# Kernel tuning notes

Hardware: AMD Instinct MI355X
Metric: run time of the kernel (lower is better)

## Reference

```python
import jax, jax.numpy as jnp
import numpy as np

N, D_IN, D_OUT, NHEAD = 4096, 512, 128, 4


def setup_inputs() -> dict:
    key = jax.random.key(0)
    k1, k2, k3, k4, k5 = jax.random.split(key, 5)
    adj = jax.random.randint(k1, (N, N), 0, 2).astype(jnp.float32)  # dense binary adjacency
    x = jax.random.normal(k2, (N, D_IN), dtype=jnp.float32)
    W = jax.random.normal(k3, (D_IN, D_OUT), dtype=jnp.float32) * (1.0 / np.sqrt(D_IN))
    attn_l_w = jax.random.normal(k4, (NHEAD, D_OUT), dtype=jnp.float32) * (1.0 / np.sqrt(D_OUT))
    attn_r_w = jax.random.normal(k5, (NHEAD, D_OUT), dtype=jnp.float32) * (1.0 / np.sqrt(D_OUT))
    b = jnp.zeros((D_OUT,), dtype=jnp.float32)
    return {"adj": adj, "x": x, "W": W, "attn_l_w": attn_l_w, "attn_r_w": attn_r_w, "b": b}


def reference(adj, x, W, attn_l_w, attn_r_w, b):
    # h = x @ W : [N, D_OUT]
    h = x @ W
    el = h @ attn_l_w.T  # [N, H]  (nn.Linear(output_dim, nhead, bias=False))
    er = h @ attn_r_w.T  # [N, H]
    # Dense equivalent of nonzero-gather + index_put_ scatter into [N, N, H]:
    # attn[i, j, :] = exp(leaky_relu(el[i] + er[j])) where adj[i, j] != 0, else 0.
    e = el[:, None, :] + er[None, :, :]                      # [N, N, H]
    a = jnp.where(adj[:, :, None] != 0,
                  jnp.exp(jax.nn.leaky_relu(e, negative_slope=0.2)),
                  jnp.zeros((), dtype=e.dtype))              # [N, N, H]
    a = jnp.transpose(a, (0, 2, 1))                          # [N, H, N]
    # F.normalize(p=1, dim=-1): divide by max(L1 row sum, 1e-12); a >= 0 so L1 = sum.
    a = a / jnp.maximum(jnp.sum(a, axis=-1, keepdims=True), 1e-12)
    out = jnp.einsum('nhm,md->nhd', a, h) + b                # [N, H, D_OUT]
    return out.reshape(out.shape[0], -1)                     # flatten heads -> [N, H*D_OUT]
```

## Files before the change

kernel.cpp:

```cpp
#include <hip/hip_runtime.h>

#define NN 4096
#define DIN 512
#define DOUT 128
#define NH 4
#define LOG2E 1.44269504088896340736f

typedef __bf16 bf16x8 __attribute__((ext_vector_type(8)));
typedef float f32x4 __attribute__((ext_vector_type(4)));
typedef unsigned short u16;
typedef u16 u16x8 __attribute__((ext_vector_type(8)));
typedef unsigned long long u64;

static __device__ __forceinline__ u16 f2bf(float f) {
  __bf16 h = (__bf16)f;
  return __builtin_bit_cast(u16, h);
}

__global__ __launch_bounds__(256) void pack_adj(const float* __restrict__ adj,
                                                u64* __restrict__ adjW) {
  const int t = threadIdx.x;
  const int lane = t & 63;
  const int wv = t >> 6;
  const size_t blk = blockIdx.x;
  #pragma unroll
  for (int it = 0; it < 4; ++it) {
    const size_t wbase = blk * 128 + it * 32 + wv * 8;
    float v[8];
    #pragma unroll
    for (int u = 0; u < 8; ++u) v[u] = adj[(wbase + u) * 64 + lane];
    #pragma unroll
    for (int u = 0; u < 8; ++u) {
      const u64 m = __ballot(v[u] != 0.0f);
      if (lane == 0) adjW[wbase + u] = m;
    }
  }
}

__global__ __launch_bounds__(256) void prep_wt(const float* __restrict__ W,
                                               u16* __restrict__ wthi,
                                               u16* __restrict__ wtlo) {
  const int n = blockIdx.x;
  const int t = threadIdx.x;
  for (int k = t; k < 512; k += 256) {
    const float w = W[(size_t)k * 128 + n];
    const __bf16 hi = (__bf16)w;
    const float lo = w - (float)hi;
    wthi[(size_t)n * 512 + k] = __builtin_bit_cast(u16, hi);
    wtlo[(size_t)n * 512 + k] = f2bf(lo);
  }
}

__global__ __launch_bounds__(256, 2) void hcompute(
    const float* __restrict__ x, const u16* __restrict__ wthi,
    const u16* __restrict__ wtlo, const float* __restrict__ alw,
    const float* __restrict__ arw, u16* __restrict__ hT,
    float* __restrict__ el, float* __restrict__ erT) {
  __shared__ __align__(16) char pool[73728];
  float* h_lds = (float*)(pool + 8192);
  const int t = threadIdx.x;
  const int i0 = blockIdx.x * 16;
  const int lane = t & 63, wv = t >> 6;
  const int l15 = lane & 15, lhi = lane >> 4;
  f32x4 acc[2];
  #pragma unroll
  for (int nt = 0; nt < 2; ++nt) acc[nt] = (f32x4){0.f, 0.f, 0.f, 0.f};
  const int xr = t >> 4, xq = (t & 15) * 8;
  const unsigned x_waddr = (unsigned)(xr * 256 + xq * 2) ^ (unsigned)((xr & 7) << 4);
  const int wn = t >> 1, wkh = (t & 1) * 64;

  for (int kc = 0; kc < 4; ++kc) {
    __syncthreads();
    {
      const float* xsrc = x + (size_t)(i0 + xr) * DIN + kc * 128 + xq;
      float xv[8];
      *(float4*)xv = *(const float4*)xsrc;
      *(float4*)(xv + 4) = *(const float4*)(xsrc + 4);
      u16x8 xhi, xlo;
      #pragma unroll
      for (int q = 0; q < 8; ++q) {
        const __bf16 hh = (__bf16)xv[q];
        xhi[q] = __builtin_bit_cast(u16, hh);
        xlo[q] = f2bf(xv[q] - (float)hh);
      }
      *(u16x8*)(pool + x_waddr) = xhi;
      *(u16x8*)(pool + 4096 + x_waddr) = xlo;
    }
    {
      const u16* whsrc = wthi + (size_t)wn * 512 + kc * 128 + wkh;
      const u16* wlsrc = wtlo + (size_t)wn * 512 + kc * 128 + wkh;
      #pragma unroll
      for (int q = 0; q < 8; ++q) {
        const unsigned addr =
            (unsigned)(wn * 256 + (wkh + q * 8) * 2) ^ (unsigned)((wn & 7) << 4);
        *(u16x8*)(pool + 8192 + addr) = *(const u16x8*)(whsrc + q * 8);
        *(u16x8*)(pool + 40960 + addr) = *(const u16x8*)(wlsrc + q * 8);
      }
    }
    __syncthreads();
    #pragma unroll
    for (int ks = 0; ks < 4; ++ks) {
      const unsigned kbyte = (unsigned)(ks * 64 + lhi * 16);
      const unsigned xoff = (unsigned)(l15 * 256) + (kbyte ^ (unsigned)((l15 & 7) << 4));
      const bf16x8 ah = *(const bf16x8*)(pool + xoff);
      const bf16x8 al = *(const bf16x8*)(pool + 4096 + xoff);
      #pragma unroll
      for (int nt = 0; nt < 2; ++nt) {
        const int n = wv * 32 + nt * 16 + l15;
        const unsigned wb = (unsigned)(n * 256) + (kbyte ^ (unsigned)((n & 7) << 4));
        const bf16x8 bh = *(const bf16x8*)(pool + 8192 + wb);
        const bf16x8 bl = *(const bf16x8*)(pool + 40960 + wb);
        acc[nt] = __builtin_amdgcn_mfma_f32_16x16x32_bf16(ah, bh, acc[nt], 0, 0, 0);
        acc[nt] = __builtin_amdgcn_mfma_f32_16x16x32_bf16(al, bh, acc[nt], 0, 0, 0);
        acc[nt] = __builtin_amdgcn_mfma_f32_16x16x32_bf16(ah, bl, acc[nt], 0, 0, 0);
      }
    }
  }
  __syncthreads();
  #pragma unroll
  for (int nt = 0; nt < 2; ++nt)
    #pragma unroll
    for (int reg = 0; reg < 4; ++reg)
      h_lds[(lhi * 4 + reg) * 132 + wv * 32 + nt * 16 + l15] = acc[nt][reg];
  __syncthreads();
  {
    const int d = t >> 1, ih = (t & 1) * 8;
    u16x8 hv;
    #pragma unroll
    for (int q = 0; q < 8; ++q) hv[q] = f2bf(h_lds[(ih + q) * 132 + d]);
    *(u16x8*)(hT + (size_t)d * NN + i0 + ih) = hv;
  }
  if (t < 128) {
    const int r = t >> 3, hh = (t >> 1) & 3, side = t & 1;
    const float* wrow = (side ? arw : alw) + hh * DOUT;
    float s = 0.f;
    for (int d = 0; d < 128; ++d) s += h_lds[r * 132 + d] * wrow[d];
    s *= LOG2E;
    if (side == 0) el[(size_t)(i0 + r) * NH + hh] = s;
    else erT[(size_t)hh * NN + i0 + r] = s;
  }
}

template <int KSPLIT>
__global__ __launch_bounds__(512, 4) void gat_main(
    const unsigned char* __restrict__ adjB, const u16* __restrict__ hT,
    const float* __restrict__ el, const float* __restrict__ erT,
    const float* __restrict__ bias, float* __restrict__ outp,
    float* __restrict__ accP, float* __restrict__ SP) {
  constexpr int NIT = 64 / KSPLIT;
  __shared__ __align__(16) u16 A_lds[2][64 * 64];
  __shared__ __align__(16) u16 B_lds[2][128 * 64];
  __shared__ float S_lds[64];
  const int t = threadIdx.x;
  const int b = blockIdx.x;
  const int g = b & 255;
  const int ks = (KSPLIT > 1) ? (b >> 8) : 0;
  const int i0 = g * 16;
  const int row = t >> 3, head = row >> 4, il = row & 15;
  const int j0 = (t & 7) * 8;
  const float elv = el[(size_t)(i0 + il) * NH + head];
  const unsigned char* adjrow =
      adjB + (size_t)(i0 + il) * 512 + (size_t)ks * NIT * 8 + (t & 7);
  const float* errow = erT + (size_t)head * NN + ks * NIT * 64 + j0;
  const unsigned a_off = (unsigned)(row * 128 + j0 * 2) ^ (unsigned)((row & 7) << 4);
  const int bd = t >> 3, bk0 = (t & 7) * 8;
  const u16* hrow = hT + (size_t)bd * NN + ks * NIT * 64 + bk0;
  const unsigned b_off0 = (unsigned)(bd * 128 + bk0 * 2) ^ (unsigned)((bd & 7) << 4);
  const unsigned b_off1 =
      (unsigned)((bd + 64) * 128 + bk0 * 2) ^ (unsigned)((bd & 7) << 4);
  const int lane = t & 63, w = t >> 6;
  const int rt = w >> 1, ch = w & 1;
  const int l15 = lane & 15, lhi = lane >> 4;
  const int am = rt * 16 + l15;
  const unsigned aswz = (unsigned)((am & 7) << 4);
  f32x4 acc[4];
  #pragma unroll
  for (int ct = 0; ct < 4; ++ct) acc[ct] = (f32x4){0.f, 0.f, 0.f, 0.f};
  float Sp = 0.f;

  auto genTile = [&](unsigned char abv, const float4& ea, const float4& eb,
                     char* Abuf, char* Bbuf, const u16x8& h0, const u16x8& h1) {
    float ev[8];
    *(float4*)ev = ea;
    *(float4*)(ev + 4) = eb;
    u16x8 pk;
    float s = 0.f;
    #pragma unroll
    for (int q = 0; q < 8; ++q) {
      const float e = elv + ev[q];
      const float ex = exp2f(fmaxf(e, 0.f) + 0.2f * fminf(e, 0.f));
      const float av = (float)((abv >> q) & 1) * ex;
      s += av;
      pk[q] = f2bf(av);
    }
    Sp += s;
    *(u16x8*)(Abuf + a_off) = pk;
    *(u16x8*)(Bbuf + b_off0) = h0;
    *(u16x8*)(Bbuf + b_off1) = h1;
  };

  {
    const unsigned char ab = adjrow[0];
    const float4 e0 = *(const float4*)errow;
    const float4 e1 = *(const float4*)(errow + 4);
    const u16x8 h0 = *(const u16x8*)hrow;
    const u16x8 h1 = *(const u16x8*)(hrow + (size_t)64 * NN);
    genTile(ab, e0, e1, (char*)A_lds[0], (char*)B_lds[0], h0, h1);
  }

  for (int jt = 0; jt < NIT; ++jt) {
    const int cur = jt & 1;
    __syncthreads();
    unsigned char abn = 0;
    float4 e0n, e1n;
    u16x8 h0n, h1n;
    const bool more = (jt + 1 < NIT);
    if (more) {
      abn = adjrow[(jt + 1) * 8];
      e0n = *(const float4*)(errow + (jt + 1) * 64);
      e1n = *(const float4*)(errow + (jt + 1) * 64 + 4);
      h0n = *(const u16x8*)(hrow + (jt + 1) * 64);
      h1n = *(const u16x8*)(hrow + (jt + 1) * 64 + (size_t)64 * NN);
    }
    const char* Abc = (const char*)A_lds[cur];
    const char* Bbc = (const char*)B_lds[cur];
    #pragma unroll
    for (int kk = 0; kk < 2; ++kk) {
      const unsigned kbyte = (unsigned)(kk * 64 + lhi * 16);
      const bf16x8 af = *(const bf16x8*)(Abc + (am * 128 + (kbyte ^ aswz)));
      #pragma unroll
      for (int ct = 0; ct < 4; ++ct) {
        const int col = ch * 64 + ct * 16 + l15;
        const bf16x8 bfr = *(const bf16x8*)(
            Bbc + (col * 128 + (kbyte ^ (unsigned)((col & 7) << 4))));
        acc[ct] = __builtin_amdgcn_mfma_f32_16x16x32_bf16(af, bfr, acc[ct], 0, 0, 0);
      }
    }
    if (more)
      genTile(abn, e0n, e1n, (char*)A_lds[cur ^ 1], (char*)B_lds[cur ^ 1], h0n, h1n);
  }

  Sp += __shfl_xor(Sp, 1);
  Sp += __shfl_xor(Sp, 2);
  Sp += __shfl_xor(Sp, 4);

  if (KSPLIT == 1) {
    if ((t & 7) == 0) S_lds[row] = Sp;
    __syncthreads();
    #pragma unroll
    for (int reg = 0; reg < 4; ++reg) {
      const int mrow = rt * 16 + lhi * 4 + reg;
      const float inv = 1.f / fmaxf(S_lds[mrow], 1e-12f);
      const int irow = i0 + (mrow & 15);
      #pragma unroll
      for (int ct = 0; ct < 4; ++ct) {
        const int colp = ch * 64 + ct * 16 + l15;
        outp[(size_t)irow * (NH * DOUT) + rt * DOUT + colp] =
            acc[ct][reg] * inv + bias[colp];
      }
    }
  } else {
    if ((t & 7) == 0) SP[(size_t)b * 64 + row] = Sp;
    float* dst = accP + (size_t)b * 8192;
    #pragma unroll
    for (int reg = 0; reg < 4; ++reg) {
      const int mrow = rt * 16 + lhi * 4 + reg;
      #pragma unroll
      for (int ct = 0; ct < 4; ++ct) {
        const int colp = ch * 64 + ct * 16 + l15;
        dst[mrow * 128 + colp] = acc[ct][reg];
      }
    }
  }
}

__global__ __launch_bounds__(256) void reduce_norm(
    const float* __restrict__ accP, const float* __restrict__ SP,
    const float* __restrict__ bias, float* __restrict__ outp) {
  const int idx = blockIdx.x * 256 + threadIdx.x;
  const int o = idx * 4;
  const int d = o & 127;
  const int h = (o >> 7) & 3;
  const int i = o >> 9;
  const int g = i >> 4;
  const int m = h * 16 + (i & 15);
  const float4 p0 = *(const float4*)(accP + (size_t)g * 8192 + m * 128 + d);
  const float4 p1 = *(const float4*)(accP + (size_t)(256 + g) * 8192 + m * 128 + d);
  const float S = SP[(size_t)g * 64 + m] + SP[(size_t)(256 + g) * 64 + m];
  const float inv = 1.f / fmaxf(S, 1e-12f);
  const float4 bb = *(const float4*)(bias + d);
  float4 r;
  r.x = (p0.x + p1.x) * inv + bb.x;
  r.y = (p0.y + p1.y) * inv + bb.y;
  r.z = (p0.z + p1.z) * inv + bb.z;
  r.w = (p0.w + p1.w) * inv + bb.w;
  *(float4*)(outp + o) = r;
}

extern "C" void kernel_launch(void* const* d_in, const int* in_sizes, int n_in,
                              void* d_out, int out_size, void* d_ws, size_t ws_size,
                              hipStream_t stream) {
  const float* adj = (const float*)d_in[0];
  const float* x = (const float*)d_in[1];
  const float* W = (const float*)d_in[2];
  const float* alw = (const float*)d_in[3];
  const float* arw = (const float*)d_in[4];
  const float* bias = (const float*)d_in[5];
  float* out = (float*)d_out;
  char* ws = (char*)d_ws;
  u16* hT = (u16*)ws;
  float* el = (float*)(ws + 0x100000);
  float* erT = (float*)(ws + 0x110000);
  unsigned char* adjB = (unsigned char*)(ws + 0x120000);
  u16* wthi = (u16*)(ws + 0x320000);
  u16* wtlo = (u16*)(ws + 0x340000);
  float* accP = (float*)(ws + 0x360000);
  float* SP = (float*)(ws + 0x1360000);
  const bool ksplit2 = ws_size >= 0x1380000ull;

  pack_adj<<<2048, 256, 0, stream>>>(adj, (u64*)adjB);
  prep_wt<<<128, 256, 0, stream>>>(W, wthi, wtlo);
  hcompute<<<256, 256, 0, stream>>>(x, wthi, wtlo, alw, arw, hT, el, erT);
  if (ksplit2) {
    gat_main<2><<<512, 512, 0, stream>>>(adjB, hT, el, erT, bias, out, accP, SP);
    reduce_norm<<<2048, 256, 0, stream>>>(accP, SP, bias, out);
  } else {
    gat_main<1><<<256, 512, 0, stream>>>(adjB, hT, el, erT, bias, out, accP, SP);
  }
}
```

Before: 177.3 us.

## Async global-to-LDS staging, 3-way K split, and branchless leaky-relu mask

The main GAT kernel now stages the hT tiles straight into LDS with global_load_lds instead of going through registers. It also splits the neighbour dimension three ways when the workspace allows, giving 768 blocks instead of 512 for better CU fill. Leaky-relu becomes a single fma on |e| and the adjacency mask is applied with a bitwise AND instead of a multiply. hcompute moves to 512 threads, double-buffers W through direct LDS loads, and prefetches the next x chunk. The 3-way split adds partial-sum traffic in reduce_norm and needs more workspace.

```diff
diff --git a/kernel.cpp b/kernel.cpp
--- a/kernel.cpp
+++ b/kernel.cpp
@@ -10,11 +10,18 @@
 typedef float f32x4 __attribute__((ext_vector_type(4)));
 typedef unsigned short u16;
 typedef u16 u16x8 __attribute__((ext_vector_type(8)));
+typedef u16 u16x4 __attribute__((ext_vector_type(4)));
 typedef unsigned long long u64;
 
 static __device__ __forceinline__ u16 f2bf(float f) {
   __bf16 h = (__bf16)f;
   return __builtin_bit_cast(u16, h);
+}
+
+static __device__ __forceinline__ void gl_lds16(const void* g, void* l) {
+  __builtin_amdgcn_global_load_lds(
+      (const __attribute__((address_space(1))) unsigned int*)g,
+      (__attribute__((address_space(3))) unsigned int*)l, 16, 0, 0);
 }
 
 __global__ __launch_bounds__(256) void pack_adj(const float* __restrict__ adj,
@@ -51,84 +58,92 @@
   }
 }
 
-__global__ __launch_bounds__(256, 2) void hcompute(
+__global__ __launch_bounds__(512, 1) void hcompute(
     const float* __restrict__ x, const u16* __restrict__ wthi,
     const u16* __restrict__ wtlo, const float* __restrict__ alw,
     const float* __restrict__ arw, u16* __restrict__ hT,
     float* __restrict__ el, float* __restrict__ erT) {
-  __shared__ __align__(16) char pool[73728];
-  float* h_lds = (float*)(pool + 8192);
+  __shared__ __align__(16) char pool[147456];
   const int t = threadIdx.x;
   const int i0 = blockIdx.x * 16;
-  const int lane = t & 63, wv = t >> 6;
+  const int lane = t & 63, w = t >> 6;
   const int l15 = lane & 15, lhi = lane >> 4;
-  f32x4 acc[2];
-  #pragma unroll
-  for (int nt = 0; nt < 2; ++nt) acc[nt] = (f32x4){0.f, 0.f, 0.f, 0.f};
-  const int xr = t >> 4, xq = (t & 15) * 8;
-  const unsigned x_waddr = (unsigned)(xr * 256 + xq * 2) ^ (unsigned)((xr & 7) << 4);
-  const int wn = t >> 1, wkh = (t & 1) * 64;
-
+
+  const int xr = t >> 5, xk = (t & 31) * 4;
+  const unsigned x_off =
+      ((unsigned)(xr * 256 + xk * 2)) ^ ((unsigned)((xr & 7) << 4));
+
+  f32x4 acc = (f32x4){0.f, 0.f, 0.f, 0.f};
+
+  auto stageW = [&](int kc, int buf) {
+    #pragma unroll
+    for (int q = 0; q < 4; ++q) {
+      const int off = q * 8192 + t * 16;
+      const int n = off >> 8;
+      const int kb = off & 255;
+      const int ksrc = (kb ^ ((n & 7) << 4)) >> 1;
+      const size_t so = (size_t)n * 512 + kc * 128 + ksrc;
+      gl_lds16(wthi + so, pool + 16384 + buf * 32768 + off);
+      gl_lds16(wtlo + so, pool + 81920 + buf * 32768 + off);
+    }
+  };
+  auto writeX = [&](const float4& xv, int buf) {
+    u16x4 hi, lo;
+    const float* xp = (const float*)&xv;
+    #pragma unroll
+    for (int j = 0; j < 4; ++j) {
+      const __bf16 hb = (__bf16)xp[j];
+      hi[j] = __builtin_bit_cast(u16, hb);
+      lo[j] = f2bf(xp[j] - (float)hb);
+    }
+    *(u16x4*)(pool + buf * 4096 + x_off) = hi;
+    *(u16x4*)(pool + 8192 + buf * 4096 + x_off) = lo;
+  };
+
+  stageW(0, 0);
+  {
+    float4 xv = *(const float4*)(x + (size_t)(i0 + xr) * DIN + xk);
+    writeX(xv, 0);
+  }
+  float4 xnext;
   for (int kc = 0; kc < 4; ++kc) {
+    const int cur = kc & 1;
     __syncthreads();
-    {
-      const float* xsrc = x + (size_t)(i0 + xr) * DIN + kc * 128 + xq;
-      float xv[8];
-      *(float4*)xv = *(const float4*)xsrc;
-      *(float4*)(xv + 4) = *(const float4*)(xsrc + 4);
-      u16x8 xhi, xlo;
-      #pragma unroll
-      for (int q = 0; q < 8; ++q) {
-        const __bf16 hh = (__bf16)xv[q];
-        xhi[q] = __builtin_bit_cast(u16, hh);
-        xlo[q] = f2bf(xv[q] - (float)hh);
-      }
-      *(u16x8*)(pool + x_waddr) = xhi;
-      *(u16x8*)(pool + 4096 + x_waddr) = xlo;
-    }
-    {
-      const u16* whsrc = wthi + (size_t)wn * 512 + kc * 128 + wkh;
-      const u16* wlsrc = wtlo + (size_t)wn * 512 + kc * 128 + wkh;
-      #pragma unroll
-      for (int q = 0; q < 8; ++q) {
-        const unsigned addr =
-            (unsigned)(wn * 256 + (wkh + q * 8) * 2) ^ (unsigned)((wn & 7) << 4);
-        *(u16x8*)(pool + 8192 + addr) = *(const u16x8*)(whsrc + q * 8);
-        *(u16x8*)(pool + 40960 + addr) = *(const u16x8*)(wlsrc + q * 8);
-      }
-    }
-    __syncthreads();
+    const bool more = (kc < 3);
+    if (more) {
+      stageW(kc + 1, cur ^ 1);
+      xnext = *(const float4*)(x + (size_t)(i0 + xr) * DIN + (kc + 1) * 128 + xk);
+    }
     #pragma unroll
     for (int ks = 0; ks < 4; ++ks) {
       const unsigned kbyte = (unsigned)(ks * 64 + lhi * 16);
-      const unsigned xoff = (unsigned)(l15 * 256) + (kbyte ^ (unsigned)((l15 & 7) << 4));
-      const bf16x8 ah = *(const bf16x8*)(pool + xoff);
-      const bf16x8 al = *(const bf16x8*)(pool + 4096 + xoff);
-      #pragma unroll
-      for (int nt = 0; nt < 2; ++nt) {
-        const int n = wv * 32 + nt * 16 + l15;
-        const unsigned wb = (unsigned)(n * 256) + (kbyte ^ (unsigned)((n & 7) << 4));
-        const bf16x8 bh = *(const bf16x8*)(pool + 8192 + wb);
-        const bf16x8 bl = *(const bf16x8*)(pool + 40960 + wb);
-        acc[nt] = __builtin_amdgcn_mfma_f32_16x16x32_bf16(ah, bh, acc[nt], 0, 0, 0);
-        acc[nt] = __builtin_amdgcn_mfma_f32_16x16x32_bf16(al, bh, acc[nt], 0, 0, 0);
-        acc[nt] = __builtin_amdgcn_mfma_f32_16x16x32_bf16(ah, bl, acc[nt], 0, 0, 0);
-      }
-    }
+      const unsigned xoff =
+          (unsigned)(l15 * 256) + (kbyte ^ (unsigned)((l15 & 7) << 4));
+      const bf16x8 ah = *(const bf16x8*)(pool + cur * 4096 + xoff);
+      const bf16x8 al = *(const bf16x8*)(pool + 8192 + cur * 4096 + xoff);
+      const int n = w * 16 + l15;
+      const unsigned wb =
+          (unsigned)(n * 256) + (kbyte ^ (unsigned)((n & 7) << 4));
+      const bf16x8 bh = *(const bf16x8*)(pool + 16384 + cur * 32768 + wb);
+      const bf16x8 bl = *(const bf16x8*)(pool + 81920 + cur * 32768 + wb);
+      acc = __builtin_amdgcn_mfma_f32_16x16x32_bf16(ah, bh, acc, 0, 0, 0);
+      acc = __builtin_amdgcn_mfma_f32_16x16x32_bf16(al, bh, acc, 0, 0, 0);
+      acc = __builtin_amdgcn_mfma_f32_16x16x32_bf16(ah, bl, acc, 0, 0, 0);
+    }
+    if (more) writeX(xnext, cur ^ 1);
   }
   __syncthreads();
+  float* h_lds = (float*)(pool + 16384);
   #pragma unroll
-  for (int nt = 0; nt < 2; ++nt)
-    #pragma unroll
-    for (int reg = 0; reg < 4; ++reg)
-      h_lds[(lhi * 4 + reg) * 132 + wv * 32 + nt * 16 + l15] = acc[nt][reg];
+  for (int reg = 0; reg < 4; ++reg)
+    h_lds[(lhi * 4 + reg) * 132 + w * 16 + l15] = acc[reg];
   __syncthreads();
   {
-    const int d = t >> 1, ih = (t & 1) * 8;
-    u16x8 hv;
-    #pragma unroll
-    for (int q = 0; q < 8; ++q) hv[q] = f2bf(h_lds[(ih + q) * 132 + d]);
-    *(u16x8*)(hT + (size_t)d * NN + i0 + ih) = hv;
+    const int d = t >> 2, ih0 = (t & 3) * 4;
+    u16x4 hv;
+    #pragma unroll
+    for (int j = 0; j < 4; ++j) hv[j] = f2bf(h_lds[(ih0 + j) * 132 + d]);
+    *(u16x4*)(hT + (size_t)d * NN + i0 + ih0) = hv;
   }
   if (t < 128) {
     const int r = t >> 3, hh = (t >> 1) & 3, side = t & 1;
@@ -147,7 +162,6 @@
     const float* __restrict__ el, const float* __restrict__ erT,
     const float* __restrict__ bias, float* __restrict__ outp,
     float* __restrict__ accP, float* __restrict__ SP) {
-  constexpr int NIT = 64 / KSPLIT;
   __shared__ __align__(16) u16 A_lds[2][64 * 64];
   __shared__ __align__(16) u16 B_lds[2][128 * 64];
   __shared__ float S_lds[64];
@@ -156,18 +170,18 @@
   const int g = b & 255;
   const int ks = (KSPLIT > 1) ? (b >> 8) : 0;
   const int i0 = g * 16;
+  const int jbeg = (ks * 64) / KSPLIT;
+  const int jcnt = ((ks + 1) * 64) / KSPLIT - jbeg;
   const int row = t >> 3, head = row >> 4, il = row & 15;
-  const int j0 = (t & 7) * 8;
   const float elv = el[(size_t)(i0 + il) * NH + head];
-  const unsigned char* adjrow =
-      adjB + (size_t)(i0 + il) * 512 + (size_t)ks * NIT * 8 + (t & 7);
-  const float* errow = erT + (size_t)head * NN + ks * NIT * 64 + j0;
-  const unsigned a_off = (unsigned)(row * 128 + j0 * 2) ^ (unsigned)((row & 7) << 4);
-  const int bd = t >> 3, bk0 = (t & 7) * 8;
-  const u16* hrow = hT + (size_t)bd * NN + ks * NIT * 64 + bk0;
-  const unsigned b_off0 = (unsigned)(bd * 128 + bk0 * 2) ^ (unsigned)((bd & 7) << 4);
-  const unsigned b_off1 =
-      (unsigned)((bd + 64) * 128 + bk0 * 2) ^ (unsigned)((bd & 7) << 4);
+  const unsigned char* adjrow = adjB + (size_t)(i0 + il) * 512 + jbeg * 8 + (t & 7);
+  const float* errow = erT + (size_t)head * NN + jbeg * 64 + (t & 7) * 8;
+  const unsigned a_off =
+      (unsigned)(row * 128 + (t & 7) * 16) ^ (unsigned)((row & 7) << 4);
+  const int bd = t >> 3;
+  const int bkb = (t & 7) * 16;
+  const u16* hsrc = hT + (size_t)bd * NN + jbeg * 64 +
+                    (((unsigned)bkb ^ (unsigned)((bd & 7) << 4)) >> 1);
   const int lane = t & 63, w = t >> 6;
   const int rt = w >> 1, ch = w & 1;
   const int l15 = lane & 15, lhi = lane >> 4;
@@ -178,8 +192,12 @@
   for (int ct = 0; ct < 4; ++ct) acc[ct] = (f32x4){0.f, 0.f, 0.f, 0.f};
   float Sp = 0.f;
 
-  auto genTile = [&](unsigned char abv, const float4& ea, const float4& eb,
-                     char* Abuf, char* Bbuf, const u16x8& h0, const u16x8& h1) {
+  auto stageB = [&](int jt, int buf) {
+    char* dst = (char*)B_lds[buf] + t * 16;
+    gl_lds16(hsrc + jt * 64, dst);
+    gl_lds16(hsrc + jt * 64 + (size_t)64 * NN, dst + 8192);
+  };
+  auto genA = [&](unsigned char abv, const float4& ea, const float4& eb, int buf) {
     float ev[8];
     *(float4*)ev = ea;
     *(float4*)(ev + 4) = eb;
@@ -188,39 +206,36 @@
     #pragma unroll
     for (int q = 0; q < 8; ++q) {
       const float e = elv + ev[q];
-      const float ex = exp2f(fmaxf(e, 0.f) + 0.2f * fminf(e, 0.f));
-      const float av = (float)((abv >> q) & 1) * ex;
+      const float l = fmaf(0.4f, __builtin_fabsf(e), 0.6f * e);
+      const float ex = exp2f(l);
+      const int msk = ((int)((unsigned)abv << (31 - q))) >> 31;
+      const float av = __builtin_bit_cast(float, __builtin_bit_cast(int, ex) & msk);
       s += av;
       pk[q] = f2bf(av);
     }
     Sp += s;
-    *(u16x8*)(Abuf + a_off) = pk;
-    *(u16x8*)(Bbuf + b_off0) = h0;
-    *(u16x8*)(Bbuf + b_off1) = h1;
+    *(u16x8*)((char*)A_lds[buf] + a_off) = pk;
   };
 
+  stageB(0, 0);
   {
     const unsigned char ab = adjrow[0];
     const float4 e0 = *(const float4*)errow;
     const float4 e1 = *(const float4*)(errow + 4);
-    const u16x8 h0 = *(const u16x8*)hrow;
-    const u16x8 h1 = *(const u16x8*)(hrow + (size_t)64 * NN);
-    genTile(ab, e0, e1, (char*)A_lds[0], (char*)B_lds[0], h0, h1);
-  }
-
-  for (int jt = 0; jt < NIT; ++jt) {
+    genA(ab, e0, e1, 0);
+  }
+
+  for (int jt = 0; jt < jcnt; ++jt) {
     const int cur = jt & 1;
     __syncthreads();
+    const bool more = (jt + 1 < jcnt);
     unsigned char abn = 0;
-    float4 e0n, e1n;
-    u16x8 h0n, h1n;
-    const bool more = (jt + 1 < NIT);
+    float4 e0n = {0, 0, 0, 0}, e1n = {0, 0, 0, 0};
     if (more) {
+      stageB(jt + 1, cur ^ 1);
       abn = adjrow[(jt + 1) * 8];
       e0n = *(const float4*)(errow + (jt + 1) * 64);
       e1n = *(const float4*)(errow + (jt + 1) * 64 + 4);
-      h0n = *(const u16x8*)(hrow + (jt + 1) * 64);
-      h1n = *(const u16x8*)(hrow + (jt + 1) * 64 + (size_t)64 * NN);
     }
     const char* Abc = (const char*)A_lds[cur];
     const char* Bbc = (const char*)B_lds[cur];
@@ -236,8 +251,7 @@
         acc[ct] = __builtin_amdgcn_mfma_f32_16x16x32_bf16(af, bfr, acc[ct], 0, 0, 0);
       }
     }
-    if (more)
-      genTile(abn, e0n, e1n, (char*)A_lds[cur ^ 1], (char*)B_lds[cur ^ 1], h0n, h1n);
+    if (more) genA(abn, e0n, e1n, cur ^ 1);
   }
 
   Sp += __shfl_xor(Sp, 1);
@@ -274,26 +288,33 @@
   }
 }
 
+template <int KS>
 __global__ __launch_bounds__(256) void reduce_norm(
     const float* __restrict__ accP, const float* __restrict__ SP,
     const float* __restrict__ bias, float* __restrict__ outp) {
   const int idx = blockIdx.x * 256 + threadIdx.x;
   const int o = idx * 4;
   const int d = o & 127;
-  const int h = (o >> 7) & 3;
+  const int hh = (o >> 7) & 3;
   const int i = o >> 9;
   const int g = i >> 4;
-  const int m = h * 16 + (i & 15);
-  const float4 p0 = *(const float4*)(accP + (size_t)g * 8192 + m * 128 + d);
-  const float4 p1 = *(const float4*)(accP + (size_t)(256 + g) * 8192 + m * 128 + d);
-  const float S = SP[(size_t)g * 64 + m] + SP[(size_t)(256 + g) * 64 + m];
+  const int m = hh * 16 + (i & 15);
+  float4 p = make_float4(0.f, 0.f, 0.f, 0.f);
+  float S = 0.f;
+  #pragma unroll
+  for (int s = 0; s < KS; ++s) {
+    const float4 q =
+        *(const float4*)(accP + (size_t)(s * 256 + g) * 8192 + m * 128 + d);
+    p.x += q.x; p.y += q.y; p.z += q.z; p.w += q.w;
+    S += SP[(size_t)(s * 256 + g) * 64 + m];
+  }
   const float inv = 1.f / fmaxf(S, 1e-12f);
   const float4 bb = *(const float4*)(bias + d);
   float4 r;
-  r.x = (p0.x + p1.x) * inv + bb.x;
-  r.y = (p0.y + p1.y) * inv + bb.y;
-  r.z = (p0.z + p1.z) * inv + bb.z;
-  r.w = (p0.w + p1.w) * inv + bb.w;
+  r.x = p.x * inv + bb.x;
+  r.y = p.y * inv + bb.y;
+  r.z = p.z * inv + bb.z;
+  r.w = p.w * inv + bb.w;
   *(float4*)(outp + o) = r;
 }
 
@@ -315,16 +336,21 @@
   u16* wthi = (u16*)(ws + 0x320000);
   u16* wtlo = (u16*)(ws + 0x340000);
   float* accP = (float*)(ws + 0x360000);
-  float* SP = (float*)(ws + 0x1360000);
-  const bool ksplit2 = ws_size >= 0x1380000ull;
+  const size_t need3 = 0x360000ull + 768ull * 32768 + 768ull * 256;
+  const size_t need2 = 0x360000ull + 512ull * 32768 + 512ull * 256;
 
   pack_adj<<<2048, 256, 0, stream>>>(adj, (u64*)adjB);
   prep_wt<<<128, 256, 0, stream>>>(W, wthi, wtlo);
-  hcompute<<<256, 256, 0, stream>>>(x, wthi, wtlo, alw, arw, hT, el, erT);
-  if (ksplit2) {
+  hcompute<<<256, 512, 0, stream>>>(x, wthi, wtlo, alw, arw, hT, el, erT);
+  if (ws_size >= need3) {
+    float* SP = (float*)(ws + 0x360000 + 768ull * 32768);
+    gat_main<3><<<768, 512, 0, stream>>>(adjB, hT, el, erT, bias, out, accP, SP);
+    reduce_norm<3><<<2048, 256, 0, stream>>>(accP, SP, bias, out);
+  } else if (ws_size >= need2) {
+    float* SP = (float*)(ws + 0x360000 + 512ull * 32768);
     gat_main<2><<<512, 512, 0, stream>>>(adjB, hT, el, erT, bias, out, accP, SP);
-    reduce_norm<<<2048, 256, 0, stream>>>(accP, SP, bias, out);
+    reduce_norm<2><<<2048, 256, 0, stream>>>(accP, SP, bias, out);
   } else {
-    gat_main<1><<<256, 512, 0, stream>>>(adjB, hT, el, erT, bias, out, accP, SP);
-  }
-}
+    gat_main<1><<<256, 512, 0, stream>>>(adjB, hT, el, erT, bias, out, accP, accP);
+  }
+}
```

Result: faster. 170.3 us (-3.9%).
